# Kernel tuning notes

Hardware: AMD Instinct MI355X
Metric: run time of the kernel (lower is better)

Reference implementation:

```python
import jax, jax.numpy as jnp
import numpy as np

NUM_HEADS = 8
NUM_KEY_FEATURES = 128  # 32*1 + 32*3 (key fiber num_features)
N_NODES = 50000
N_EDGES = 500000
CH = 32  # value/key channels per degree


def setup_inputs() -> dict:
    key = jax.random.key(0)
    ks = jax.random.split(key, 7)
    return {
        "key0": jax.random.normal(ks[0], (N_EDGES, CH, 1), jnp.float32),
        "key1": jax.random.normal(ks[1], (N_EDGES, CH, 3), jnp.float32),
        "value0": jax.random.normal(ks[2], (N_EDGES, CH, 1), jnp.float32),
        "value1": jax.random.normal(ks[3], (N_EDGES, CH, 3), jnp.float32),
        "query0": jax.random.normal(ks[4], (N_NODES, CH, 1), jnp.float32),
        "query1": jax.random.normal(ks[5], (N_NODES, CH, 3), jnp.float32),
        "dst": jax.random.randint(ks[6], (N_EDGES,), 0, N_NODES, jnp.int64),
    }


def _to_heads(d0, d1):
    # Fiber.to_attention_heads: per-degree [*, C, 2d+1] -> [*, H, C//H*(2d+1)], concat over degrees
    a = d0.reshape(d0.shape[0], NUM_HEADS, -1)
    b = d1.reshape(d1.shape[0], NUM_HEADS, -1)
    return jnp.concatenate([a, b], axis=-1)  # [*, H, 16]


def reference(key0, key1, value0, value1, query0, query1, dst):
    n_nodes = query0.shape[0]
    k = _to_heads(key0, key1)      # [E, H, F]
    q = _to_heads(query0, query1)  # [N, H, F]
    # dgl.ops.e_dot_v: dot(key_e, query_{dst(e)}) per head
    logits = jnp.einsum('ehf,ehf->eh', k, q[dst]) / np.sqrt(NUM_KEY_FEATURES).astype(np.float32)
    # edge_softmax over incoming edges of each dst node
    m = jax.ops.segment_max(logits, dst, num_segments=n_nodes)       # [N, H]
    ex = jnp.exp(logits - m[dst])                                    # [E, H]
    s = jax.ops.segment_sum(ex, dst, num_segments=n_nodes)          # [N, H]
    w = ex / s[dst]                                                  # [E, H]

    def agg(v):
        e, c, dd = v.shape
        vh = v.reshape(e, NUM_HEADS, c // NUM_HEADS, dd)
        wv = w[:, :, None, None] * vh                                # [E, H, C/H, 2d+1]
        out = jax.ops.segment_sum(wv, dst, num_segments=n_nodes)
        return out.reshape(n_nodes, c, dd)                           # [N, C, 2d+1]

    return agg(value0), agg(value1)
```

## Files before the change

kernel.cpp:

```cpp
#include <hip/hip_runtime.h>
#include <hip/hip_bf16.h>
#include <math.h>

#define NHEADS 8
#define CHVAL 32
#define SCB 1024
#define WPB 4

__global__ void hist_kernel(const int* __restrict__ dst, int* __restrict__ cnt, int E) {
    int e = blockIdx.x * blockDim.x + threadIdx.x;
    if (e < E) atomicAdd(&cnt[dst[e]], 1);
}

__global__ void scan1_kernel(int* __restrict__ cnt, int* __restrict__ btot, int N) {
    __shared__ int sh[SCB];
    int t = threadIdx.x;
    int i = blockIdx.x * SCB + t;
    int v = (i < N) ? cnt[i] : 0;
    sh[t] = v;
    __syncthreads();
    for (int off = 1; off < SCB; off <<= 1) {
        int y = (t >= off) ? sh[t - off] : 0;
        __syncthreads();
        sh[t] += y;
        __syncthreads();
    }
    if (i < N) cnt[i] = sh[t] - v;
    if (t == SCB - 1) btot[blockIdx.x] = sh[t];
}

__global__ void scan2_kernel(int* __restrict__ btot, int nb) {
    __shared__ int sh[64];
    int t = threadIdx.x;
    int v = (t < nb) ? btot[t] : 0;
    sh[t] = v;
    __syncthreads();
    for (int off = 1; off < 64; off <<= 1) {
        int y = (t >= off) ? sh[t - off] : 0;
        __syncthreads();
        sh[t] += y;
        __syncthreads();
    }
    if (t < nb) btot[t] = sh[t] - v;
}

__global__ void scan3_kernel(const int* __restrict__ cnt, const int* __restrict__ btot,
                             int* __restrict__ offs, int* __restrict__ cursor,
                             int N, int E) {
    int i = blockIdx.x * blockDim.x + threadIdx.x;
    if (i < N) {
        int o = cnt[i] + btot[i >> 10];
        offs[i] = o;
        cursor[i] = o;
    }
    if (i == 0) offs[N] = E;
}

__global__ void scatter_kernel(const int* __restrict__ dst,
                               int* __restrict__ cursor,
                               int* __restrict__ eid,
                               int E) {
    int e = blockIdx.x * blockDim.x + threadIdx.x;
    if (e < E) {
        int pos = atomicAdd(&cursor[dst[e]], 1);
        eid[pos] = e;
    }
}

__global__ void __launch_bounds__(64 * WPB)
node_fused_kernel(const float4* __restrict__ key0,
                  const float4* __restrict__ key1,
                  const float4* __restrict__ q0,
                  const float4* __restrict__ q1,
                  const float4* __restrict__ value0,
                  const float4* __restrict__ value1,
                  const int* __restrict__ offs,
                  const int* __restrict__ eid,
                  float4* __restrict__ out0,
                  float4* __restrict__ out1,
                  int N) {
    __shared__ float w_sh[WPB][64][9];
    __shared__ int   e_sh[WPB][64];
    __shared__ float scale_sh[WPB][8];

    int wv = threadIdx.x >> 6;
    int t  = threadIdx.x & 63;
    int n  = blockIdx.x * WPB + wv;
    if (n >= N) return;

    int beg = offs[n];
    int deg = offs[n + 1] - beg;

    if (deg == 0) {
        float4 z = {0.f, 0.f, 0.f, 0.f};
        if (t < 8) out0[(size_t)n * 8 + t] = z;
        else if (t < 32) out1[(size_t)n * 24 + (t - 8)] = z;
        return;
    }

    const float SCALE = 0.08838834764831845f;
    int s = t >> 3;
    int h = t & 7;

    float4 qa  = q0[(size_t)n * 8 + h];
    float4 qb0 = q1[(size_t)n * 24 + 3 * h + 0];
    float4 qb1 = q1[(size_t)n * 24 + 3 * h + 1];
    float4 qb2 = q1[(size_t)n * 24 + 3 * h + 2];

    int half = t >> 5;
    int l = t & 31;
    int myh = (l < 8) ? l : ((l - 8) / 3);

    float m_run = -INFINITY;
    float s_run = 0.0f;
    float4 acc = {0.f, 0.f, 0.f, 0.f};

    for (int base = 0; base < deg; base += 64) {
        int clen = min(64, deg - base);

        float lgreg[8];
#pragma unroll
        for (int r = 0; r < 8; ++r) {
            int slot = base + r * 8 + s;
            float lg = -INFINITY;
            if (slot < deg) {
                int e = eid[beg + slot];
                if (h == 0) e_sh[wv][r * 8 + s] = e;
                float4 ka  = key0[(size_t)e * 8 + h];
                float4 kb0 = key1[(size_t)e * 24 + 3 * h + 0];
                float4 kb1 = key1[(size_t)e * 24 + 3 * h + 1];
                float4 kb2 = key1[(size_t)e * 24 + 3 * h + 2];
                float d = ka.x * qa.x + ka.y * qa.y + ka.z * qa.z + ka.w * qa.w
                        + kb0.x * qb0.x + kb0.y * qb0.y + kb0.z * qb0.z + kb0.w * qb0.w
                        + kb1.x * qb1.x + kb1.y * qb1.y + kb1.z * qb1.z + kb1.w * qb1.w
                        + kb2.x * qb2.x + kb2.y * qb2.y + kb2.z * qb2.z + kb2.w * qb2.w;
                lg = d * SCALE;
            }
            lgreg[r] = lg;
        }

        float cm = lgreg[0];
#pragma unroll
        for (int r = 1; r < 8; ++r) cm = fmaxf(cm, lgreg[r]);
        cm = fmaxf(cm, __shfl_xor(cm, 8, 64));
        cm = fmaxf(cm, __shfl_xor(cm, 16, 64));
        cm = fmaxf(cm, __shfl_xor(cm, 32, 64));

        float new_m = fmaxf(m_run, cm);
        float rescale = __expf(m_run - new_m);

        float chsum = 0.0f;
#pragma unroll
        for (int r = 0; r < 8; ++r) chsum += __expf(lgreg[r] - new_m);
        chsum += __shfl_xor(chsum, 8, 64);
        chsum += __shfl_xor(chsum, 16, 64);
        chsum += __shfl_xor(chsum, 32, 64);

        s_run = s_run * rescale + chsum;
        m_run = new_m;

#pragma unroll
        for (int r = 0; r < 8; ++r)
            w_sh[wv][r * 8 + s][h] = __expf(lgreg[r] - new_m);
        if (t < 8) scale_sh[wv][t] = rescale;
        __builtin_amdgcn_wave_barrier();

        float rs = scale_sh[wv][myh];
        acc.x *= rs; acc.y *= rs; acc.z *= rs; acc.w *= rs;

        for (int ii = half; ii < clen; ii += 2) {
            int e = e_sh[wv][ii];
            float w = w_sh[wv][ii][myh];
            float4 v = (l < 8) ? value0[(size_t)e * 8 + l]
                               : value1[(size_t)e * 24 + (l - 8)];
            acc.x += w * v.x;
            acc.y += w * v.y;
            acc.z += w * v.z;
            acc.w += w * v.w;
        }
        __builtin_amdgcn_wave_barrier();
    }

    if (t < 8) scale_sh[wv][t] = 1.0f / s_run;
    __builtin_amdgcn_wave_barrier();
    float inv = scale_sh[wv][myh];
    acc.x *= inv; acc.y *= inv; acc.z *= inv; acc.w *= inv;

    acc.x += __shfl_xor(acc.x, 32, 64);
    acc.y += __shfl_xor(acc.y, 32, 64);
    acc.z += __shfl_xor(acc.z, 32, 64);
    acc.w += __shfl_xor(acc.w, 32, 64);
    if (t < 8)       out0[(size_t)n * 8 + l] = acc;
    else if (t < 32) out1[(size_t)n * 24 + (l - 8)] = acc;
}

extern "C" void kernel_launch(void* const* d_in, const int* in_sizes, int n_in,
                              void* d_out, int out_size, void* d_ws, size_t ws_size,
                              hipStream_t stream) {
    const float* key0   = (const float*)d_in[0];
    const float* key1   = (const float*)d_in[1];
    const float* value0 = (const float*)d_in[2];
    const float* value1 = (const float*)d_in[3];
    const float* query0 = (const float*)d_in[4];
    const float* query1 = (const float*)d_in[5];
    const int*   dst    = (const int*)d_in[6];

    int E = in_sizes[0] / CHVAL;
    int N = in_sizes[4] / CHVAL;
    int nb = (N + SCB - 1) / SCB;

    int* cnt    = (int*)d_ws;
    int* offs   = cnt + N;
    int* cursor = offs + N + 1;
    int* eid    = cursor + N;
    int* btot   = eid + E;

    float* out0 = (float*)d_out;
    float* out1 = out0 + (size_t)N * 32;

    hipMemsetAsync(cnt, 0, (size_t)N * sizeof(int), stream);

    int blk = 256;
    hist_kernel<<<(E + blk - 1) / blk, blk, 0, stream>>>(dst, cnt, E);

    scan1_kernel<<<nb, SCB, 0, stream>>>(cnt, btot, N);
    scan2_kernel<<<1, 64, 0, stream>>>(btot, nb);
    scan3_kernel<<<(N + blk - 1) / blk, blk, 0, stream>>>(cnt, btot, offs, cursor, N, E);

    scatter_kernel<<<(E + blk - 1) / blk, blk, 0, stream>>>(dst, cursor, eid, E);

    int nnb = (N + WPB - 1) / WPB;
    node_fused_kernel<<<nnb, 64 * WPB, 0, stream>>>(
        (const float4*)key0, (const float4*)key1,
        (const float4*)query0, (const float4*)query1,
        (const float4*)value0, (const float4*)value1,
        offs, eid,
        (float4*)out0, (float4*)out1, N);
}
```

Measured before the change: 194.0 us.

## Map eight lanes per node with per-lane online softmax, dropping shared memory

Each destination node is now handled by 8 lanes instead of a full 64-lane wave, so one wave processes 8 nodes. Each lane owns one head and keeps its own running max, sum and four float4 accumulators, which removes the shared-memory staging, cross-lane shuffles and wave barriers. Edges are walked in chunks of 16 with online softmax rescaling. This should waste fewer lanes on low-degree nodes (average degree is about 10), but it brings divergence across the 8 nodes of a wave when their degrees differ, more registers per lane, and edge ids read twice.

```diff
diff --git a/kernel.cpp b/kernel.cpp
--- a/kernel.cpp
+++ b/kernel.cpp
@@ -5,7 +5,6 @@
 #define NHEADS 8
 #define CHVAL 32
 #define SCB 1024
-#define WPB 4
 
 __global__ void hist_kernel(const int* __restrict__ dst, int* __restrict__ cnt, int E) {
     int e = blockIdx.x * blockDim.x + threadIdx.x;
@@ -67,7 +66,7 @@
     }
 }
 
-__global__ void __launch_bounds__(64 * WPB)
+__global__ void __launch_bounds__(256)
 node_fused_kernel(const float4* __restrict__ key0,
                   const float4* __restrict__ key1,
                   const float4* __restrict__ q0,
@@ -79,13 +78,12 @@
                   float4* __restrict__ out0,
                   float4* __restrict__ out1,
                   int N) {
-    __shared__ float w_sh[WPB][64][9];
-    __shared__ int   e_sh[WPB][64];
-    __shared__ float scale_sh[WPB][8];
-
-    int wv = threadIdx.x >> 6;
-    int t  = threadIdx.x & 63;
-    int n  = blockIdx.x * WPB + wv;
+    int t = threadIdx.x;
+    int lane = t & 63;
+    int wv = t >> 6;
+    int g = lane >> 3;
+    int j = lane & 7;
+    int n = (blockIdx.x * 4 + wv) * 8 + g;
     if (n >= N) return;
 
     int beg = offs[n];
@@ -93,105 +91,87 @@
 
     if (deg == 0) {
         float4 z = {0.f, 0.f, 0.f, 0.f};
-        if (t < 8) out0[(size_t)n * 8 + t] = z;
-        else if (t < 32) out1[(size_t)n * 24 + (t - 8)] = z;
+        out0[(size_t)n * 8 + j] = z;
+        out1[(size_t)n * 24 + 3 * j + 0] = z;
+        out1[(size_t)n * 24 + 3 * j + 1] = z;
+        out1[(size_t)n * 24 + 3 * j + 2] = z;
         return;
     }
 
     const float SCALE = 0.08838834764831845f;
-    int s = t >> 3;
-    int h = t & 7;
-
-    float4 qa  = q0[(size_t)n * 8 + h];
-    float4 qb0 = q1[(size_t)n * 24 + 3 * h + 0];
-    float4 qb1 = q1[(size_t)n * 24 + 3 * h + 1];
-    float4 qb2 = q1[(size_t)n * 24 + 3 * h + 2];
-
-    int half = t >> 5;
-    int l = t & 31;
-    int myh = (l < 8) ? l : ((l - 8) / 3);
-
-    float m_run = -INFINITY;
-    float s_run = 0.0f;
-    float4 acc = {0.f, 0.f, 0.f, 0.f};
-
-    for (int base = 0; base < deg; base += 64) {
-        int clen = min(64, deg - base);
-
-        float lgreg[8];
+
+    float4 qa  = q0[(size_t)n * 8 + j];
+    float4 qb0 = q1[(size_t)n * 24 + 3 * j + 0];
+    float4 qb1 = q1[(size_t)n * 24 + 3 * j + 1];
+    float4 qb2 = q1[(size_t)n * 24 + 3 * j + 2];
+
+    float m = -INFINITY;
+    float s = 0.0f;
+    float4 a0 = {0.f, 0.f, 0.f, 0.f};
+    float4 a1 = {0.f, 0.f, 0.f, 0.f};
+    float4 a2 = {0.f, 0.f, 0.f, 0.f};
+    float4 a3 = {0.f, 0.f, 0.f, 0.f};
+
+    for (int cb = 0; cb < deg; cb += 16) {
+        float lg[16];
+        float cmax = -INFINITY;
 #pragma unroll
-        for (int r = 0; r < 8; ++r) {
-            int slot = base + r * 8 + s;
-            float lg = -INFINITY;
+        for (int i = 0; i < 16; ++i) {
+            lg[i] = -INFINITY;
+            int slot = cb + i;
             if (slot < deg) {
                 int e = eid[beg + slot];
-                if (h == 0) e_sh[wv][r * 8 + s] = e;
-                float4 ka  = key0[(size_t)e * 8 + h];
-                float4 kb0 = key1[(size_t)e * 24 + 3 * h + 0];
-                float4 kb1 = key1[(size_t)e * 24 + 3 * h + 1];
-                float4 kb2 = key1[(size_t)e * 24 + 3 * h + 2];
+                float4 ka  = key0[(size_t)e * 8 + j];
+                float4 kb0 = key1[(size_t)e * 24 + 3 * j + 0];
+                float4 kb1 = key1[(size_t)e * 24 + 3 * j + 1];
+                float4 kb2 = key1[(size_t)e * 24 + 3 * j + 2];
                 float d = ka.x * qa.x + ka.y * qa.y + ka.z * qa.z + ka.w * qa.w
                         + kb0.x * qb0.x + kb0.y * qb0.y + kb0.z * qb0.z + kb0.w * qb0.w
                         + kb1.x * qb1.x + kb1.y * qb1.y + kb1.z * qb1.z + kb1.w * qb1.w
                         + kb2.x * qb2.x + kb2.y * qb2.y + kb2.z * qb2.z + kb2.w * qb2.w;
-                lg = d * SCALE;
+                lg[i] = d * SCALE;
             }
-            lgreg[r] = lg;
+            cmax = fmaxf(cmax, lg[i]);
         }
 
-        float cm = lgreg[0];
+        float nm = fmaxf(m, cmax);
+        float rs = __expf(m - nm);
+        s *= rs;
+        a0.x *= rs; a0.y *= rs; a0.z *= rs; a0.w *= rs;
+        a1.x *= rs; a1.y *= rs; a1.z *= rs; a1.w *= rs;
+        a2.x *= rs; a2.y *= rs; a2.z *= rs; a2.w *= rs;
+        a3.x *= rs; a3.y *= rs; a3.z *= rs; a3.w *= rs;
+
 #pragma unroll
-        for (int r = 1; r < 8; ++r) cm = fmaxf(cm, lgreg[r]);
-        cm = fmaxf(cm, __shfl_xor(cm, 8, 64));
-        cm = fmaxf(cm, __shfl_xor(cm, 16, 64));
-        cm = fmaxf(cm, __shfl_xor(cm, 32, 64));
-
-        float new_m = fmaxf(m_run, cm);
-        float rescale = __expf(m_run - new_m);
-
-        float chsum = 0.0f;
-#pragma unroll
-        for (int r = 0; r < 8; ++r) chsum += __expf(lgreg[r] - new_m);
-        chsum += __shfl_xor(chsum, 8, 64);
-        chsum += __shfl_xor(chsum, 16, 64);
-        chsum += __shfl_xor(chsum, 32, 64);
-
-        s_run = s_run * rescale + chsum;
-        m_run = new_m;
-
-#pragma unroll
-        for (int r = 0; r < 8; ++r)
-            w_sh[wv][r * 8 + s][h] = __expf(lgreg[r] - new_m);
-        if (t < 8) scale_sh[wv][t] = rescale;
-        __builtin_amdgcn_wave_barrier();
-
-        float rs = scale_sh[wv][myh];
-        acc.x *= rs; acc.y *= rs; acc.z *= rs; acc.w *= rs;
-
-        for (int ii = half; ii < clen; ii += 2) {
-            int e = e_sh[wv][ii];
-            float w = w_sh[wv][ii][myh];
-            float4 v = (l < 8) ? value0[(size_t)e * 8 + l]
-                               : value1[(size_t)e * 24 + (l - 8)];
-            acc.x += w * v.x;
-            acc.y += w * v.y;
-            acc.z += w * v.z;
-            acc.w += w * v.w;
+        for (int i = 0; i < 16; ++i) {
+            int slot = cb + i;
+            float w = __expf(lg[i] - nm);
+            s += w;
+            if (slot < deg) {
+                int e = eid[beg + slot];
+                float4 v0 = value0[(size_t)e * 8 + j];
+                float4 w0 = value1[(size_t)e * 24 + 3 * j + 0];
+                float4 w1 = value1[(size_t)e * 24 + 3 * j + 1];
+                float4 w2 = value1[(size_t)e * 24 + 3 * j + 2];
+                a0.x += w * v0.x; a0.y += w * v0.y; a0.z += w * v0.z; a0.w += w * v0.w;
+                a1.x += w * w0.x; a1.y += w * w0.y; a1.z += w * w0.z; a1.w += w * w0.w;
+                a2.x += w * w1.x; a2.y += w * w1.y; a2.z += w * w1.z; a2.w += w * w1.w;
+                a3.x += w * w2.x; a3.y += w * w2.y; a3.z += w * w2.z; a3.w += w * w2.w;
+            }
         }
-        __builtin_amdgcn_wave_barrier();
-    }
-
-    if (t < 8) scale_sh[wv][t] = 1.0f / s_run;
-    __builtin_amdgcn_wave_barrier();
-    float inv = scale_sh[wv][myh];
-    acc.x *= inv; acc.y *= inv; acc.z *= inv; acc.w *= inv;
-
-    acc.x += __shfl_xor(acc.x, 32, 64);
-    acc.y += __shfl_xor(acc.y, 32, 64);
-    acc.z += __shfl_xor(acc.z, 32, 64);
-    acc.w += __shfl_xor(acc.w, 32, 64);
-    if (t < 8)       out0[(size_t)n * 8 + l] = acc;
-    else if (t < 32) out1[(size_t)n * 24 + (l - 8)] = acc;
+        m = nm;
+    }
+
+    float inv = 1.0f / s;
+    a0.x *= inv; a0.y *= inv; a0.z *= inv; a0.w *= inv;
+    a1.x *= inv; a1.y *= inv; a1.z *= inv; a1.w *= inv;
+    a2.x *= inv; a2.y *= inv; a2.z *= inv; a2.w *= inv;
+    a3.x *= inv; a3.y *= inv; a3.z *= inv; a3.w *= inv;
+
+    out0[(size_t)n * 8 + j] = a0;
+    out1[(size_t)n * 24 + 3 * j + 0] = a1;
+    out1[(size_t)n * 24 + 3 * j + 1] = a2;
+    out1[(size_t)n * 24 + 3 * j + 2] = a3;
 }
 
 extern "C" void kernel_launch(void* const* d_in, const int* in_sizes, int n_in,
@@ -229,8 +209,9 @@
 
     scatter_kernel<<<(E + blk - 1) / blk, blk, 0, stream>>>(dst, cursor, eid, E);
 
-    int nnb = (N + WPB - 1) / WPB;
-    node_fused_kernel<<<nnb, 64 * WPB, 0, stream>>>(
+    int nwaves = (N + 7) / 8;
+    int nblocks = (nwaves + 3) / 4;
+    node_fused_kernel<<<nblocks, 256, 0, stream>>>(
         (const float4*)key0, (const float4*)key1,
         (const float4*)query0, (const float4*)query1,
         (const float4*)value0, (const float4*)value1,
```

Measured after the change: 207.2 us. +6.8%, slower.
